# Kernel optimization log

Measured on AMD Instinct MI355X. Metric: run time of the kernel, lower is better.

## Reference

```python
import jax, jax.numpy as jnp
import numpy as np
import math

B = 2
H = 16
M = 1024
D = 64      # head_dim
P = 1024    # persistent memory size
SPAN = 1024 # external attention span


def setup_inputs() -> dict:
    key = jax.random.key(0)
    k1, k2, k3, k4 = jax.random.split(key, 4)
    query = jax.random.normal(k1, (B * H, M, D), dtype=jnp.float32)
    attn = jax.random.normal(k2, (B * H, M, SPAN), dtype=jnp.float32)
    # params as in __init__
    pkey = jax.random.normal(k3, (H, D, P), dtype=jnp.float32) / math.sqrt(D)
    pval = jax.random.normal(k4, (H, P, D), dtype=jnp.float32) / math.sqrt(P)
    return {"query": query, "attn": attn, "key": pkey, "val": pval}


def reference(query, attn, key, val):
    h, d, p = key.shape
    bh, m, _ = query.shape
    q = query.reshape(-1, h, m, d)                      # [B,H,M,D]
    # attn_pers = q @ (key * sqrt(d)); later divided by sqrt(d) -> net q@key
    attn_pers = jnp.einsum('bhmd,hdp->bhmp', q, key * math.sqrt(d))
    attn_pers = attn_pers.reshape(-1, m, p)             # [B*H,M,P]
    scores = jnp.concatenate([attn, attn_pers], axis=-1) / math.sqrt(d)
    probs = jax.nn.softmax(scores, axis=-1)             # [B*H,M,SPAN+P]
    attn_out = probs[:, :, :-p]                         # [B*H,M,SPAN]
    pers = probs[:, :, -p:].reshape(-1, h, m, p)        # [B,H,M,P]
    out = jnp.einsum('bhmp,hpd->bhmd', pers, val * math.sqrt(p))
    out = out.reshape(-1, m, d)                         # [B*H,M,D]
    return (attn_out, out)
```

## Files before the change

### kernel.cpp

```cpp
#include <hip/hip_runtime.h>
#include <hip/hip_bf16.h>
#include <math.h>

#define BH   32
#define NH   16
#define MM   1024
#define DD   64
#define PP   1024
#define SPAN 1024

typedef unsigned short ushort_t;
typedef __attribute__((ext_vector_type(8))) short  short8;
typedef __attribute__((ext_vector_type(4))) float  f32x4;

#define MFMA(a,b,c) __builtin_amdgcn_mfma_f32_16x16x32_bf16(a,b,c,0,0,0)

#define WS_MIZ_OFF (8388608ull)
#define WS_NEED    (8388608ull + 262144ull)

__device__ __forceinline__ ushort_t f2bf(float x) {
    __hip_bfloat16 b = __float2bfloat16(x);
    return __builtin_bit_cast(unsigned short, b);
}
__device__ __forceinline__ float bf2f(ushort_t u) {
    __hip_bfloat16 b = __builtin_bit_cast(__hip_bfloat16, u);
    return __bfloat162float(b);
}

__launch_bounds__(256)
__global__ void pm_pre(const float* __restrict__ key,
                       const float* __restrict__ val,
                       ushort_t* __restrict__ wsKV)
{
    int bi = blockIdx.x, t = threadIdx.x;
    if (bi < 512) {
        int id = bi * 256 + t;
        int l  = id & 63;
        int ks = (id >> 6) & 1;
        int pb = (id >> 7) & 3;
        int c  = (id >> 9) & 15;
        int h  = id >> 13;
        int p     = c * 64 + pb * 16 + (l & 15);
        int dbase = ks * 32 + (l >> 4) * 8;
        size_t fo = (size_t)(h * 16 + c) * 16384 + (size_t)(pb * 2 + ks) * 1024 + (size_t)l * 8;
#pragma unroll
        for (int e = 0; e < 8; ++e) {
            float x = key[(size_t)(h * 64 + dbase + e) * PP + p];
            ushort_t hh = f2bf(x);
            wsKV[fo + e]       = hh;
            wsKV[fo + 512 + e] = f2bf(x - bf2f(hh));
        }
    } else {
        int id = (bi - 512) * 256 + t;
        int l   = id & 63;
        int db  = (id >> 6) & 3;
        int ks2 = (id >> 8) & 1;
        int c   = (id >> 9) & 15;
        int h   = id >> 13;
        int d = db * 16 + (l & 15);
        size_t fo = (size_t)(h * 16 + c) * 16384 + 8192 + (size_t)(ks2 * 4 + db) * 1024 + (size_t)l * 8;
#pragma unroll
        for (int e = 0; e < 8; ++e) {
            int p = c * 64 + ks2 * 32 + ((l >> 4) * 4) + (e & 3) + 16 * (e >> 2);
            float x = val[(size_t)(h * PP + p) * DD + d];
            ushort_t hh = f2bf(x);
            wsKV[fo + e]       = hh;
            wsKV[fo + 512 + e] = f2bf(x - bf2f(hh));
        }
    }
}

__launch_bounds__(512)
__global__ void pm_main(const float* __restrict__ q,
                        const float* __restrict__ attn,
                        const ushort_t* __restrict__ wsKV,
                        float* __restrict__ ws_MiZ,
                        float* __restrict__ out)
{
    __shared__ ushort_t kvbuf[2][16384];
    __shared__ float lds_mx[64], lds_sm[64];

    const int t  = threadIdx.x;
    const int w  = t >> 6;
    const int l  = t & 63;
    const int bi = blockIdx.x;
    const int bh   = bi & 31;
    const int tile = bi >> 5;
    const int h  = bh & (NH - 1);
    const int hi = l >> 4;
    const int lo = l & 15;

    if (w < 4) {
        const int m0 = tile * 64 + w * 16;

        short8 qf[2][2];
        {
            const float* qr = q + ((size_t)bh * MM + m0 + lo) * DD + hi * 8;
#pragma unroll
            for (int ks = 0; ks < 2; ++ks) {
                float4 a = *(const float4*)(qr + ks * 32);
                float4 b = *(const float4*)(qr + ks * 32 + 4);
                float f[8] = {a.x, a.y, a.z, a.w, b.x, b.y, b.z, b.w};
                short8 qh, ql;
#pragma unroll
                for (int e = 0; e < 8; ++e) {
                    ushort_t hh = f2bf(f[e]);
                    qh[e] = (short)hh;
                    ql[e] = (short)f2bf(f[e] - bf2f(hh));
                }
                qf[ks][0] = qh;
                qf[ks][1] = ql;
            }
        }

        const ushort_t* KVb = wsKV + (size_t)h * (16 * 16384);

        auto STAGE = [&](int b, int c) {
            const char* src = (const char*)(KVb + (size_t)c * 16384) + w * 8192 + l * 16;
            char* dst = (char*)&kvbuf[b][0] + w * 8192;
#pragma unroll
            for (int j = 0; j < 8; ++j)
                __builtin_amdgcn_global_load_lds(
                    (const __attribute__((address_space(1))) void*)(src + j * 1024),
                    (__attribute__((address_space(3))) void*)(dst + j * 1024),
                    16, 0, 0);
        };

        f32x4 oacc[4] = {{0.f,0.f,0.f,0.f},{0.f,0.f,0.f,0.f},{0.f,0.f,0.f,0.f},{0.f,0.f,0.f,0.f}};
        float m_run = -INFINITY, s_run = 0.f;

        STAGE(0, 0);
        __syncthreads();

        for (int c = 0; c < 16; ++c) {
            const int cur = c & 1;
            if (c < 15) STAGE(cur ^ 1, c + 1);

            const ushort_t* Kc = &kvbuf[cur][0];
            const ushort_t* Vc = Kc + 8192;

            f32x4 sacc[4] = {{0.f,0.f,0.f,0.f},{0.f,0.f,0.f,0.f},{0.f,0.f,0.f,0.f},{0.f,0.f,0.f,0.f}};
            __builtin_amdgcn_s_setprio(1);
#pragma unroll
            for (int pb = 0; pb < 4; ++pb) {
#pragma unroll
                for (int ks = 0; ks < 2; ++ks) {
                    const ushort_t* fp = Kc + (pb * 2 + ks) * 1024 + l * 8;
                    short8 khi = *(const short8*)fp;
                    short8 klo = *(const short8*)(fp + 512);
                    sacc[pb] = MFMA(khi, qf[ks][0], sacc[pb]);
                    sacc[pb] = MFMA(khi, qf[ks][1], sacc[pb]);
                    sacc[pb] = MFMA(klo, qf[ks][0], sacc[pb]);
                }
            }
            __builtin_amdgcn_s_setprio(0);

            float cm = -INFINITY;
#pragma unroll
            for (int pb = 0; pb < 4; ++pb)
#pragma unroll
                for (int r = 0; r < 4; ++r) cm = fmaxf(cm, sacc[pb][r]);
            cm = fmaxf(cm, __shfl_xor(cm, 16));
            cm = fmaxf(cm, __shfl_xor(cm, 32));
            float mnew = fmaxf(m_run, cm);

            float ep[4][4];
            float csum = 0.f;
#pragma unroll
            for (int pb = 0; pb < 4; ++pb)
#pragma unroll
                for (int r = 0; r < 4; ++r) {
                    float e = __expf(sacc[pb][r] - mnew);
                    ep[pb][r] = e;
                    csum += e;
                }
            csum += __shfl_xor(csum, 16);
            csum += __shfl_xor(csum, 32);

            if (__all(cm <= m_run)) {
                s_run += csum;
            } else {
                float fac = __expf(m_run - mnew);
                s_run = s_run * fac + csum;
                m_run = mnew;
                float fr[4];
#pragma unroll
                for (int r = 0; r < 4; ++r) fr[r] = __shfl(fac, hi * 4 + r);
#pragma unroll
                for (int db = 0; db < 4; ++db)
#pragma unroll
                    for (int r = 0; r < 4; ++r) oacc[db][r] *= fr[r];
            }

#pragma unroll
            for (int ks2 = 0; ks2 < 2; ++ks2) {
                short8 phi8, plo8;
#pragma unroll
                for (int e = 0; e < 8; ++e) {
                    float pv = ep[ks2 * 2 + (e >> 2)][e & 3];
                    ushort_t hh = f2bf(pv);
                    phi8[e] = (short)hh;
                    plo8[e] = (short)f2bf(pv - bf2f(hh));
                }
                __builtin_amdgcn_s_setprio(1);
#pragma unroll
                for (int db = 0; db < 4; ++db) {
                    const ushort_t* vp = Vc + (ks2 * 4 + db) * 1024 + l * 8;
                    short8 vhi = *(const short8*)vp;
                    short8 vlo = *(const short8*)(vp + 512);
                    oacc[db] = MFMA(phi8, vhi, oacc[db]);
                    oacc[db] = MFMA(plo8, vhi, oacc[db]);
                    oacc[db] = MFMA(phi8, vlo, oacc[db]);
                }
                __builtin_amdgcn_s_setprio(0);
            }

            __syncthreads();
        }

        float mx = lds_mx[w * 16 + lo];
        float sm = lds_sm[w * 16 + lo];
        float M  = fmaxf(mx, m_run);
        float Z  = sm * __expf(mx - M) + s_run * __expf(m_run - M);
        float iZ = 1.f / Z;
        float fac = 32.f * __expf(m_run - M) * iZ;

        if (hi == 0) {
            size_t row = (size_t)bh * MM + m0 + lo;
            ws_MiZ[row * 2]     = M;
            ws_MiZ[row * 2 + 1] = iZ;
        }

        float fr[4];
#pragma unroll
        for (int r = 0; r < 4; ++r) fr[r] = __shfl(fac, hi * 4 + r);
#pragma unroll
        for (int reg = 0; reg < 4; ++reg) {
            size_t ro = ((size_t)bh * MM + m0 + hi * 4 + reg) * DD + lo;
#pragma unroll
            for (int db = 0; db < 4; ++db)
                __builtin_nontemporal_store(oacc[db][reg] * fr[reg], &out[ro + db * 16]);
        }
    } else {
        const int sw = w - 4;
        __syncthreads();
        for (int c = 0; c < 16; ++c) {
            const int m = tile * 64 + sw * 16 + c;
            const f32x4* arow = (const f32x4*)(attn + ((size_t)bh * MM + m) * SPAN);
            f32x4 av[4];
#pragma unroll
            for (int j = 0; j < 4; ++j) av[j] = arow[j * 64 + l];
            float mx = -INFINITY;
#pragma unroll
            for (int j = 0; j < 4; ++j) {
                av[j] *= 0.125f;
                mx = fmaxf(mx, fmaxf(fmaxf(av[j][0], av[j][1]), fmaxf(av[j][2], av[j][3])));
            }
#pragma unroll
            for (int s = 1; s < 64; s <<= 1) mx = fmaxf(mx, __shfl_xor(mx, s));
            float sm = 0.f;
#pragma unroll
            for (int j = 0; j < 4; ++j)
#pragma unroll
                for (int e = 0; e < 4; ++e) sm += __expf(av[j][e] - mx);
#pragma unroll
            for (int s = 1; s < 64; s <<= 1) sm += __shfl_xor(sm, s);
            if (l == 0) { lds_mx[sw * 16 + c] = mx; lds_sm[sw * 16 + c] = sm; }
            __syncthreads();
        }
    }
}

__launch_bounds__(256)
__global__ void pm_norm(const float* __restrict__ attn,
                        const float* __restrict__ ws_MiZ,
                        float* __restrict__ attn_out)
{
    const int t = threadIdx.x;
    const int w = t >> 6;
    const int l = t & 63;
    const size_t row = (size_t)blockIdx.x * 4 + w;

    const float2 mz = ((const float2*)ws_MiZ)[row];
    const float M = mz.x, iZ = mz.y;

    const f32x4* arow = (const f32x4*)(attn + row * SPAN);
    f32x4*       orow = (f32x4*)(attn_out + row * SPAN);
#pragma unroll
    for (int j = 0; j < 4; ++j) {
        f32x4 a = arow[j * 64 + l];
        f32x4 o;
#pragma unroll
        for (int e = 0; e < 4; ++e) o[e] = __expf(a[e] * 0.125f - M) * iZ;
        __builtin_nontemporal_store(o, orow + j * 64 + l);
    }
}

__launch_bounds__(256)
__global__ void pm_fallback(const float* __restrict__ q,
                            const float* __restrict__ attn,
                            const float* __restrict__ key,
                            const float* __restrict__ val,
                            float* __restrict__ attn_out,
                            float* __restrict__ out)
{
    __shared__ float qs[64][68];
    __shared__ float ks[64][68];
    __shared__ float vs[64][DD];
    __shared__ float sc[64][66];
    __shared__ float rmax[64];
    __shared__ float rsum[64];

    const int t    = threadIdx.x;
    const int bh   = blockIdx.y;
    const int tile = blockIdx.x;
    const int h    = bh & (NH - 1);
    const int m0   = tile * 64;
    const int tr   = t >> 4;
    const int tc   = t & 15;
    const int r0   = tr * 4;
    const int c0   = tc * 4;
    const int lane = t & 63;
    const int wave = t >> 6;

    const size_t qbase = (size_t)bh * MM * DD + (size_t)m0 * DD;
    const size_t abase = (size_t)bh * MM * SPAN + (size_t)m0 * SPAN;
    const size_t kbase = (size_t)h * DD * PP;
    const size_t vbase = (size_t)h * PP * DD;

#pragma unroll
    for (int j = 0; j < 16; ++j) {
        int idx = j * 256 + t;
        int r = idx >> 6, d = idx & 63;
        qs[r][d] = q[qbase + (size_t)r * DD + d];
    }
    for (int rr = 0; rr < 16; ++rr) {
        int r = wave * 16 + rr;
        const float* arow = attn + abase + (size_t)r * SPAN;
        float av[16];
        float mx = -INFINITY;
#pragma unroll
        for (int j = 0; j < 16; ++j) { av[j] = arow[j * 64 + lane] * 0.125f; mx = fmaxf(mx, av[j]); }
#pragma unroll
        for (int s = 32; s; s >>= 1) mx = fmaxf(mx, __shfl_xor(mx, s));
        float sm = 0.f;
#pragma unroll
        for (int j = 0; j < 16; ++j) sm += __expf(av[j] - mx);
#pragma unroll
        for (int s = 32; s; s >>= 1) sm += __shfl_xor(sm, s);
        if (lane == 0) { rmax[r] = mx; rsum[r] = sm; }
    }
    __syncthreads();
    for (int p0 = 0; p0 < PP; p0 += 64) {
        if (p0) __syncthreads();
#pragma unroll
        for (int j = 0; j < 16; ++j) {
            int idx = j * 256 + t;
            int d = idx >> 6, pc = idx & 63;
            ks[pc][d] = key[kbase + (size_t)d * PP + p0 + pc];
        }
        __syncthreads();
        float acc[4][4] = {};
#pragma unroll
        for (int d0 = 0; d0 < DD; d0 += 4) {
            float4 q4[4], k4[4];
#pragma unroll
            for (int rr = 0; rr < 4; ++rr) q4[rr] = *(const float4*)&qs[r0 + rr][d0];
#pragma unroll
            for (int cc = 0; cc < 4; ++cc) k4[cc] = *(const float4*)&ks[c0 + cc][d0];
#pragma unroll
            for (int rr = 0; rr < 4; ++rr)
#pragma unroll
                for (int cc = 0; cc < 4; ++cc)
                    acc[rr][cc] += q4[rr].x * k4[cc].x + q4[rr].y * k4[cc].y
                                 + q4[rr].z * k4[cc].z + q4[rr].w * k4[cc].w;
        }
#pragma unroll
        for (int rr = 0; rr < 4; ++rr) {
            float mx = fmaxf(fmaxf(acc[rr][0], acc[rr][1]), fmaxf(acc[rr][2], acc[rr][3]));
#pragma unroll
            for (int s = 8; s; s >>= 1) mx = fmaxf(mx, __shfl_xor(mx, s));
            float sm = 0.f;
#pragma unroll
            for (int cc = 0; cc < 4; ++cc) sm += __expf(acc[rr][cc] - mx);
#pragma unroll
            for (int s = 8; s; s >>= 1) sm += __shfl_xor(sm, s);
            if (tc == 0) {
                int r = r0 + rr;
                float om = rmax[r], os = rsum[r];
                float nm = fmaxf(om, mx);
                rsum[r] = os * __expf(om - nm) + sm * __expf(mx - nm);
                rmax[r] = nm;
            }
        }
    }
    __syncthreads();
    for (int rr = 0; rr < 16; ++rr) {
        int r = wave * 16 + rr;
        float Mx = rmax[r];
        float iZ = 1.0f / rsum[r];
        const float* arow = attn + abase + (size_t)r * SPAN;
        float* orow = attn_out + abase + (size_t)r * SPAN;
#pragma unroll
        for (int j = 0; j < 16; ++j) {
            float a = arow[j * 64 + lane] * 0.125f;
            orow[j * 64 + lane] = __expf(a - Mx) * iZ;
        }
    }
    float acc2[4][4] = {};
    for (int p0 = 0; p0 < PP; p0 += 64) {
        __syncthreads();
#pragma unroll
        for (int j = 0; j < 16; ++j) {
            int idx = j * 256 + t;
            int d = idx >> 6, pc = idx & 63;
            ks[pc][d] = key[kbase + (size_t)d * PP + p0 + pc];
        }
#pragma unroll
        for (int j = 0; j < 16; ++j) {
            int idx = j * 256 + t;
            int pc = idx >> 6, d = idx & 63;
            vs[pc][d] = val[vbase + (size_t)(p0 + pc) * DD + d];
        }
        __syncthreads();
        float acc[4][4] = {};
#pragma unroll
        for (int d0 = 0; d0 < DD; d0 += 4) {
            float4 q4[4], k4[4];
#pragma unroll
            for (int rr = 0; rr < 4; ++rr) q4[rr] = *(const float4*)&qs[r0 + rr][d0];
#pragma unroll
            for (int cc = 0; cc < 4; ++cc) k4[cc] = *(const float4*)&ks[c0 + cc][d0];
#pragma unroll
            for (int rr = 0; rr < 4; ++rr)
#pragma unroll
                for (int cc = 0; cc < 4; ++cc)
                    acc[rr][cc] += q4[rr].x * k4[cc].x + q4[rr].y * k4[cc].y
                                 + q4[rr].z * k4[cc].z + q4[rr].w * k4[cc].w;
        }
#pragma unroll
        for (int rr = 0; rr < 4; ++rr) {
            float Mx = rmax[r0 + rr];
#pragma unroll
            for (int cc = 0; cc < 4; ++cc)
                sc[r0 + rr][c0 + cc] = __expf(acc[rr][cc] - Mx);
        }
        __syncthreads();
        for (int pc = 0; pc < 64; ++pc) {
            float4 v4 = *(const float4*)&vs[pc][tc * 4];
#pragma unroll
            for (int rr = 0; rr < 4; ++rr) {
                float pr = sc[r0 + rr][pc];
                acc2[rr][0] += pr * v4.x;
                acc2[rr][1] += pr * v4.y;
                acc2[rr][2] += pr * v4.z;
                acc2[rr][3] += pr * v4.w;
            }
        }
    }
#pragma unroll
    for (int rr = 0; rr < 4; ++rr) {
        int r = r0 + rr;
        float s = 32.0f / rsum[r];
        float4 o;
        o.x = acc2[rr][0] * s; o.y = acc2[rr][1] * s;
        o.z = acc2[rr][2] * s; o.w = acc2[rr][3] * s;
        *(float4*)&out[(size_t)bh * MM * DD + (size_t)(m0 + r) * DD + tc * 4] = o;
    }
}

extern "C" void kernel_launch(void* const* d_in, const int* in_sizes, int n_in,
                              void* d_out, int out_size, void* d_ws, size_t ws_size,
                              hipStream_t stream) {
    const float* q    = (const float*)d_in[0];
    const float* attn = (const float*)d_in[1];
    const float* key  = (const float*)d_in[2];
    const float* val  = (const float*)d_in[3];
    float* attn_out = (float*)d_out;
    float* out      = (float*)d_out + (size_t)BH * MM * SPAN;

    if (ws_size >= WS_NEED) {
        ushort_t* wsKV   = (ushort_t*)d_ws;
        float*    ws_MiZ = (float*)((char*)d_ws + WS_MIZ_OFF);
        pm_pre <<<1024, 256, 0, stream>>>(key, val, wsKV);
        pm_main<<<512, 512, 0, stream>>>(q, attn, wsKV, ws_MiZ, out);
        pm_norm<<<8192, 256, 0, stream>>>(attn, ws_MiZ, attn_out);
    } else {
        dim3 grid(MM / 64, BH);
        pm_fallback<<<grid, 256, 0, stream>>>(q, attn, key, val, attn_out, out);
    }
}
```

Measured before the change: 89.62 us.

## Fuse attention normalization pass into main kernel, dropping separate norm launch

Merges the separate normalization kernel into the main persistent-memory kernel. After the chunk loop, each block combines the external-span and persistent softmax statistics through shared memory, then all eight waves rewrite the block's 64 attn rows as normalized probabilities before the output tile is scaled and stored. This removes one kernel launch and the workspace round-trip for per-row max and inverse sum. The attn rows are re-read while still likely cache-resident, at the cost of a serialized epilogue inside the main kernel. A launch-bounds occupancy hint is also added.

```diff
diff --git a/kernel.cpp b/kernel.cpp
--- a/kernel.cpp
+++ b/kernel.cpp
@@ -15,8 +15,7 @@
 
 #define MFMA(a,b,c) __builtin_amdgcn_mfma_f32_16x16x32_bf16(a,b,c,0,0,0)
 
-#define WS_MIZ_OFF (8388608ull)
-#define WS_NEED    (8388608ull + 262144ull)
+#define WS_NEED (8388608ull)
 
 __device__ __forceinline__ ushort_t f2bf(float x) {
     __hip_bfloat16 b = __float2bfloat16(x);
@@ -70,15 +69,17 @@
     }
 }
 
-__launch_bounds__(512)
-__global__ void pm_main(const float* __restrict__ q,
-                        const float* __restrict__ attn,
-                        const ushort_t* __restrict__ wsKV,
-                        float* __restrict__ ws_MiZ,
-                        float* __restrict__ out)
+__launch_bounds__(512, 4)
+__global__ void pm_fused(const float* __restrict__ q,
+                         const float* __restrict__ attn,
+                         const ushort_t* __restrict__ wsKV,
+                         float* __restrict__ attn_out,
+                         float* __restrict__ out)
 {
     __shared__ ushort_t kvbuf[2][16384];
     __shared__ float lds_mx[64], lds_sm[64];
+    __shared__ float lds_pm[64], lds_ps[64];
+    __shared__ float lds_M[64],  lds_iZ[64];
 
     const int t  = threadIdx.x;
     const int w  = t >> 6;
@@ -89,51 +90,52 @@
     const int h  = bh & (NH - 1);
     const int hi = l >> 4;
     const int lo = l & 15;
-
-    if (w < 4) {
-        const int m0 = tile * 64 + w * 16;
-
-        short8 qf[2][2];
-        {
-            const float* qr = q + ((size_t)bh * MM + m0 + lo) * DD + hi * 8;
-#pragma unroll
-            for (int ks = 0; ks < 2; ++ks) {
-                float4 a = *(const float4*)(qr + ks * 32);
-                float4 b = *(const float4*)(qr + ks * 32 + 4);
-                float f[8] = {a.x, a.y, a.z, a.w, b.x, b.y, b.z, b.w};
-                short8 qh, ql;
-#pragma unroll
-                for (int e = 0; e < 8; ++e) {
-                    ushort_t hh = f2bf(f[e]);
-                    qh[e] = (short)hh;
-                    ql[e] = (short)f2bf(f[e] - bf2f(hh));
-                }
-                qf[ks][0] = qh;
-                qf[ks][1] = ql;
-            }
-        }
-
-        const ushort_t* KVb = wsKV + (size_t)h * (16 * 16384);
-
-        auto STAGE = [&](int b, int c) {
-            const char* src = (const char*)(KVb + (size_t)c * 16384) + w * 8192 + l * 16;
-            char* dst = (char*)&kvbuf[b][0] + w * 8192;
-#pragma unroll
-            for (int j = 0; j < 8; ++j)
-                __builtin_amdgcn_global_load_lds(
-                    (const __attribute__((address_space(1))) void*)(src + j * 1024),
-                    (__attribute__((address_space(3))) void*)(dst + j * 1024),
-                    16, 0, 0);
-        };
-
-        f32x4 oacc[4] = {{0.f,0.f,0.f,0.f},{0.f,0.f,0.f,0.f},{0.f,0.f,0.f,0.f},{0.f,0.f,0.f,0.f}};
-        float m_run = -INFINITY, s_run = 0.f;
-
+    const bool is_comp = (w < 4);
+    const int cw = w & 3;
+
+    const size_t rowbase = (size_t)bh * MM + tile * 64;
+
+    f32x4 oacc[4] = {{0.f,0.f,0.f,0.f},{0.f,0.f,0.f,0.f},{0.f,0.f,0.f,0.f},{0.f,0.f,0.f,0.f}};
+    float m_run = -INFINITY, s_run = 0.f;
+
+    short8 qf[2][2];
+    const ushort_t* KVb = wsKV + (size_t)h * (16 * 16384);
+
+    auto STAGE = [&](int b, int c) {
+        const char* src = (const char*)(KVb + (size_t)c * 16384) + cw * 8192 + l * 16;
+        char* dst = (char*)&kvbuf[b][0] + cw * 8192;
+#pragma unroll
+        for (int j = 0; j < 8; ++j)
+            __builtin_amdgcn_global_load_lds(
+                (const __attribute__((address_space(1))) void*)(src + j * 1024),
+                (__attribute__((address_space(3))) void*)(dst + j * 1024),
+                16, 0, 0);
+    };
+
+    if (is_comp) {
+        const float* qr = q + (rowbase + cw * 16 + lo) * DD + hi * 8;
+#pragma unroll
+        for (int ks = 0; ks < 2; ++ks) {
+            float4 a = *(const float4*)(qr + ks * 32);
+            float4 b = *(const float4*)(qr + ks * 32 + 4);
+            float f[8] = {a.x, a.y, a.z, a.w, b.x, b.y, b.z, b.w};
+            short8 qh, ql;
+#pragma unroll
+            for (int e = 0; e < 8; ++e) {
+                ushort_t hh = f2bf(f[e]);
+                qh[e] = (short)hh;
+                ql[e] = (short)f2bf(f[e] - bf2f(hh));
+            }
+            qf[ks][0] = qh;
+            qf[ks][1] = ql;
+        }
         STAGE(0, 0);
-        __syncthreads();
-
-        for (int c = 0; c < 16; ++c) {
-            const int cur = c & 1;
+    }
+    __syncthreads();
+
+    for (int c = 0; c < 16; ++c) {
+        const int cur = c & 1;
+        if (is_comp) {
             if (c < 15) STAGE(cur ^ 1, c + 1);
 
             const ushort_t* Kc = &kvbuf[cur][0];
@@ -214,39 +216,9 @@
                 }
                 __builtin_amdgcn_s_setprio(0);
             }
-
-            __syncthreads();
-        }
-
-        float mx = lds_mx[w * 16 + lo];
-        float sm = lds_sm[w * 16 + lo];
-        float M  = fmaxf(mx, m_run);
-        float Z  = sm * __expf(mx - M) + s_run * __expf(m_run - M);
-        float iZ = 1.f / Z;
-        float fac = 32.f * __expf(m_run - M) * iZ;
-
-        if (hi == 0) {
-            size_t row = (size_t)bh * MM + m0 + lo;
-            ws_MiZ[row * 2]     = M;
-            ws_MiZ[row * 2 + 1] = iZ;
-        }
-
-        float fr[4];
-#pragma unroll
-        for (int r = 0; r < 4; ++r) fr[r] = __shfl(fac, hi * 4 + r);
-#pragma unroll
-        for (int reg = 0; reg < 4; ++reg) {
-            size_t ro = ((size_t)bh * MM + m0 + hi * 4 + reg) * DD + lo;
-#pragma unroll
-            for (int db = 0; db < 4; ++db)
-                __builtin_nontemporal_store(oacc[db][reg] * fr[reg], &out[ro + db * 16]);
-        }
-    } else {
-        const int sw = w - 4;
-        __syncthreads();
-        for (int c = 0; c < 16; ++c) {
-            const int m = tile * 64 + sw * 16 + c;
-            const f32x4* arow = (const f32x4*)(attn + ((size_t)bh * MM + m) * SPAN);
+        } else {
+            const int r = (w - 4) * 16 + c;
+            const f32x4* arow = (const f32x4*)(attn + (rowbase + r) * SPAN);
             f32x4 av[4];
 #pragma unroll
             for (int j = 0; j < 4; ++j) av[j] = arow[j * 64 + l];
@@ -265,34 +237,51 @@
                 for (int e = 0; e < 4; ++e) sm += __expf(av[j][e] - mx);
 #pragma unroll
             for (int s = 1; s < 64; s <<= 1) sm += __shfl_xor(sm, s);
-            if (l == 0) { lds_mx[sw * 16 + c] = mx; lds_sm[sw * 16 + c] = sm; }
-            __syncthreads();
-        }
-    }
-}
-
-__launch_bounds__(256)
-__global__ void pm_norm(const float* __restrict__ attn,
-                        const float* __restrict__ ws_MiZ,
-                        float* __restrict__ attn_out)
-{
-    const int t = threadIdx.x;
-    const int w = t >> 6;
-    const int l = t & 63;
-    const size_t row = (size_t)blockIdx.x * 4 + w;
-
-    const float2 mz = ((const float2*)ws_MiZ)[row];
-    const float M = mz.x, iZ = mz.y;
-
-    const f32x4* arow = (const f32x4*)(attn + row * SPAN);
-    f32x4*       orow = (f32x4*)(attn_out + row * SPAN);
-#pragma unroll
-    for (int j = 0; j < 4; ++j) {
-        f32x4 a = arow[j * 64 + l];
-        f32x4 o;
-#pragma unroll
-        for (int e = 0; e < 4; ++e) o[e] = __expf(a[e] * 0.125f - M) * iZ;
-        __builtin_nontemporal_store(o, orow + j * 64 + l);
+            if (l == 0) { lds_mx[r] = mx; lds_sm[r] = sm; }
+        }
+
+        __syncthreads();
+    }
+
+    if (is_comp && hi == 0) {
+        lds_pm[cw * 16 + lo] = m_run;
+        lds_ps[cw * 16 + lo] = s_run;
+    }
+    __syncthreads();
+
+#pragma unroll
+    for (int rr = 0; rr < 8; ++rr) {
+        const int r = w * 8 + rr;
+        const float mx = lds_mx[r], sm = lds_sm[r];
+        const float pm = lds_pm[r], ps = lds_ps[r];
+        const float M  = fmaxf(mx, pm);
+        const float Z  = sm * __expf(mx - M) + ps * __expf(pm - M);
+        const float iZ = 1.f / Z;
+        if (l == 0) { lds_M[r] = M; lds_iZ[r] = iZ; }
+
+        const f32x4* arow = (const f32x4*)(attn + (rowbase + r) * SPAN);
+        f32x4*       orow = (f32x4*)(attn_out + (rowbase + r) * SPAN);
+#pragma unroll
+        for (int j = 0; j < 4; ++j) {
+            f32x4 a = arow[j * 64 + l];
+            f32x4 o;
+#pragma unroll
+            for (int e = 0; e < 4; ++e) o[e] = __expf(a[e] * 0.125f - M) * iZ;
+            __builtin_nontemporal_store(o, orow + j * 64 + l);
+        }
+    }
+    __syncthreads();
+
+    if (is_comp) {
+#pragma unroll
+        for (int reg = 0; reg < 4; ++reg) {
+            const int rl = cw * 16 + hi * 4 + reg;
+            const float sc = 32.f * __expf(lds_pm[rl] - lds_M[rl]) * lds_iZ[rl];
+            const size_t ro = (rowbase + rl) * DD + lo;
+#pragma unroll
+            for (int db = 0; db < 4; ++db)
+                __builtin_nontemporal_store(oacc[db][reg] * sc, &out[ro + db * 16]);
+        }
     }
 }
 
@@ -480,11 +469,9 @@
     float* out      = (float*)d_out + (size_t)BH * MM * SPAN;
 
     if (ws_size >= WS_NEED) {
-        ushort_t* wsKV   = (ushort_t*)d_ws;
-        float*    ws_MiZ = (float*)((char*)d_ws + WS_MIZ_OFF);
-        pm_pre <<<1024, 256, 0, stream>>>(key, val, wsKV);
-        pm_main<<<512, 512, 0, stream>>>(q, attn, wsKV, ws_MiZ, out);
-        pm_norm<<<8192, 256, 0, stream>>>(attn, ws_MiZ, attn_out);
+        ushort_t* wsKV = (ushort_t*)d_ws;
+        pm_pre  <<<1024, 256, 0, stream>>>(key, val, wsKV);
+        pm_fused<<<512, 512, 0, stream>>>(q, attn, wsKV, attn_out, out);
     } else {
         dim3 grid(MM / 64, BH);
         pm_fallback<<<grid, 256, 0, stream>>>(q, attn, key, val, attn_out, out);
```

Result: slower. 93.44 us (+4.3%).
